# Kernel optimization log

Hardware: AMD Instinct MI355X
Metric: run time of the kernel (lower is better)

The kernel has to match this reference:

```python
import jax, jax.numpy as jnp
import numpy as np

HEADS = 6
EPS = 1e-5


def _na_idx(L, k, d):
    # NATTEN-style dilated neighborhood: work within dilation cosets,
    # clamp window to stay inside the image (window shifts at borders).
    i = np.arange(L)
    g = i % d
    p = i // d
    Lg = (L - g + d - 1) // d  # coset length per position
    start = np.clip(p - k // 2, 0, Lg - k)
    j = np.arange(k)
    nbr = g[:, None] + d * (start[:, None] + j[None, :])          # [L,k] neighbor coords
    rel = (start[:, None] + j[None, :]) - p[:, None] + (k - 1)    # [L,k] rpb index in [0,2k-2]
    return jnp.asarray(nbr, jnp.int32), jnp.asarray(rel, jnp.int32)


def _na2d(x, qkv_w, qkv_b, proj_w, proj_b, rpb, heads, k, d):
    # x: [B,H,W,C] NHWC neighborhood attention with relative positional bias
    B, H, W, C = x.shape
    dh = C // heads
    scale = dh ** -0.5
    qkv = (x @ qkv_w + qkv_b).reshape(B, H, W, 3, heads, dh)
    qkv = jnp.transpose(qkv, (3, 0, 4, 1, 2, 5))  # [3,B,h,H,W,dh]
    q, kk, v = qkv[0] * scale, qkv[1], qkv[2]
    nh, rh = _na_idx(H, k, d)
    nw, rw = _na_idx(W, k, d)

    def gather(t):  # [B,h,H,W,dh] -> [B,h,H,W,k,k,dh]
        t = t[:, :, nh]              # [B,h,H,k,W,dh]
        t = t[:, :, :, :, nw]        # [B,h,H,k,W,k,dh]
        return jnp.transpose(t, (0, 1, 2, 4, 3, 5, 6))

    kn, vn = gather(kk), gather(v)
    attn = jnp.einsum('bhxyd,bhxyijd->bhxyij', q, kn)  # [B,h,H,W,k,k]
    bias = rpb[:, rh]                  # [h,H,k,2k-1]
    bias = bias[:, :, :, rw]           # [h,H,k,W,k]
    bias = jnp.transpose(bias, (0, 1, 3, 2, 4))  # [h,H,W,k,k]
    attn = attn + bias[None]
    attn = jax.nn.softmax(attn.reshape(B, heads, H, W, k * k), axis=-1)
    attn = attn.reshape(B, heads, H, W, k, k)
    out = jnp.einsum('bhxyij,bhxyijd->bhxyd', attn, vn)
    out = jnp.transpose(out, (0, 2, 3, 1, 4)).reshape(B, H, W, C)
    return out @ proj_w + proj_b


def _rln(x, w, b, m1_w, m1_b, m2_w, m2_b):
    # Revised LayerNorm: normalize over (C,H,W) per sample; meta1/meta2 are 1x1 convs on std/mean
    mean = jnp.mean(x, axis=(1, 2, 3), keepdims=True)
    std = jnp.sqrt(jnp.mean((x - mean) ** 2, axis=(1, 2, 3), keepdims=True) + EPS)
    out = (x - mean) / std * w + b
    rescale = m1_w[None, :, None, None] * std + m1_b[None, :, None, None]
    rebias = m2_w[None, :, None, None] * mean + m2_b[None, :, None, None]
    return out, rescale, rebias


def _c11(x, w, b):  # 1x1 conv on NCHW == per-pixel linear
    return jnp.einsum('bchw,oc->bohw', x, w) + b[None, :, None, None]


def _gelu(x):
    return jax.nn.gelu(x, approximate=False)


def reference(x, ln_w, ln_b, m1_w, m1_b, m2_w, m2_b, qkv1_w, qkv1_b, proj1_w, proj1_b, rpb1, qkv2_w, qkv2_b, proj2_w, proj2_b, rpb2, mlp_w1, mlp_b1, mlp_w2, mlp_b2, bn_g, bn_b, bn_m, bn_v, pa_w1, pa_b1, pa_w2, pa_b2, ca_w1, ca_b1, ca_w2, ca_b2, m2a_w1, m2a_b1, m2a_w2, m2a_b2):
    # ---- NA block 1 (kernel 7, dilation 1) ----
    sc = x
    y, rs, rb = _rln(x, ln_w, ln_b, m1_w, m1_b, m2_w, m2_b)
    a = _na2d(jnp.transpose(y, (0, 2, 3, 1)), qkv1_w, qkv1_b, proj1_w, proj1_b, rpb1, HEADS, 7, 1)
    x = sc + jnp.transpose(a, (0, 3, 1, 2)) * rs + rb
    # ---- NA block 2 (kernel 5, dilation 8) ----
    sc = x
    y, rs, rb = _rln(x, ln_w, ln_b, m1_w, m1_b, m2_w, m2_b)
    a = _na2d(jnp.transpose(y, (0, 2, 3, 1)), qkv2_w, qkv2_b, proj2_w, proj2_b, rpb2, HEADS, 5, 8)
    x = sc + jnp.transpose(a, (0, 3, 1, 2)) * rs + rb
    # ---- MLP (source reuses the pre-attn2 shortcut `sc`) ----
    y, rs, rb = _rln(x, ln_w, ln_b, m1_w, m1_b, m2_w, m2_b)
    m = _c11(jax.nn.relu(_c11(y, mlp_w1, mlp_b1)), mlp_w2, mlp_b2)
    x = sc + m * rs + rb
    # ---- BN + pixel attention + channel attention + mlp2 ----
    sc = x
    inv = jax.lax.rsqrt(bn_v + EPS)
    y = (x - bn_m[None, :, None, None]) * (inv * bn_g)[None, :, None, None] + bn_b[None, :, None, None]
    pa = jax.nn.sigmoid(_c11(_gelu(_c11(y, pa_w1, pa_b1)), pa_w2, pa_b2))  # [B,1,H,W]
    y = pa * y
    gap = jnp.mean(y, axis=(2, 3), keepdims=True)
    ca = jax.nn.sigmoid(_c11(_gelu(_c11(gap, ca_w1, ca_b1)), ca_w2, ca_b2))  # [B,C,1,1]
    y = ca * y
    y = _c11(_gelu(_c11(y, m2a_w1, m2a_b1)), m2a_w2, m2a_b2)
    return sc + y


def setup_inputs() -> dict:
    key = jax.random.key(0)
    B, C, H, W, HID = 4, 96, 64, 64, 384
    ks = iter(jax.random.split(key, 48))

    def rn(shape, s=0.02):
        return jax.random.normal(next(ks), shape, jnp.float32) * s

    d = {}
    d['x'] = jax.random.normal(next(ks), (B, C, H, W), jnp.float32)
    d['ln_w'] = jnp.ones((1, C, 1, 1), jnp.float32)
    d['ln_b'] = jnp.zeros((1, C, 1, 1), jnp.float32)
    d['m1_w'] = rn((C,)); d['m1_b'] = jnp.ones((C,), jnp.float32)
    d['m2_w'] = rn((C,)); d['m2_b'] = jnp.zeros((C,), jnp.float32)
    d['qkv1_w'] = rn((C, 3 * C)); d['qkv1_b'] = jnp.zeros((3 * C,), jnp.float32)
    d['proj1_w'] = rn((C, C)); d['proj1_b'] = jnp.zeros((C,), jnp.float32)
    d['rpb1'] = rn((HEADS, 13, 13))
    d['qkv2_w'] = rn((C, 3 * C)); d['qkv2_b'] = jnp.zeros((3 * C,), jnp.float32)
    d['proj2_w'] = rn((C, C)); d['proj2_b'] = jnp.zeros((C,), jnp.float32)
    d['rpb2'] = rn((HEADS, 9, 9))
    d['mlp_w1'] = rn((HID, C)); d['mlp_b1'] = jnp.zeros((HID,), jnp.float32)
    d['mlp_w2'] = rn((C, HID)); d['mlp_b2'] = jnp.zeros((C,), jnp.float32)
    d['bn_g'] = jnp.ones((C,), jnp.float32); d['bn_b'] = jnp.zeros((C,), jnp.float32)
    d['bn_m'] = jnp.zeros((C,), jnp.float32); d['bn_v'] = jnp.ones((C,), jnp.float32)
    d['pa_w1'] = rn((C // 8, C)); d['pa_b1'] = jnp.zeros((C // 8,), jnp.float32)
    d['pa_w2'] = rn((1, C // 8)); d['pa_b2'] = jnp.zeros((1,), jnp.float32)
    d['ca_w1'] = rn((C, C)); d['ca_b1'] = jnp.zeros((C,), jnp.float32)
    d['ca_w2'] = rn((C, C)); d['ca_b2'] = jnp.zeros((C,), jnp.float32)
    d['m2a_w1'] = rn((C, C)); d['m2a_b1'] = jnp.zeros((C,), jnp.float32)
    d['m2a_w2'] = rn((C, C)); d['m2a_b2'] = jnp.zeros((C,), jnp.float32)
    return d
```

## Files before the change

### kernel.cpp

```cpp
#include <hip/hip_runtime.h>
#include <math.h>

#define CC 96
#define NP 4096
#define NHEADS 6
#define NELEMF 393216.0f
#define EPSF 1e-5f

typedef __attribute__((ext_vector_type(8))) short bf16x8;
typedef __attribute__((ext_vector_type(4))) float f32x4;
#define MFMA16(a,b,c) __builtin_amdgcn_mfma_f32_16x16x32_bf16(a,b,c,0,0,0)

#define WQKV1  64
#define WQKV2  (WQKV1+13824)
#define WPROJ1 (WQKV2+13824)
#define WPROJ2 (WPROJ1+4608)
#define WMLP1  (WPROJ2+4608)
#define WMLP2  (WMLP1+18432)
#define WM2A1  (WMLP2+18432)
#define WM2A2  (WM2A1+4608)
#define WPA1T  (WM2A2+4608)
#define WBNS   (WPA1T+1152)
#define WCA1T  (WBNS+192)
#define WCA2T  (WCA1T+9216)
#define WS_Q   870784
#define WS_K   (WS_Q+786432)
#define WS_V   (WS_K+786432)
#define WS_ATTPM (WS_V+786432)
#define WS_X1  (WS_ATTPM+786432)
#define WS_X2  (WS_X1+1572864)
#define WS_X3  (WS_X2+1572864)
#define WS_PA  (WS_X3+1572864)
#define WS_GAP (WS_PA+16384)

__device__ __forceinline__ float gelu_f(float x){
  return 0.5f * x * (1.0f + erff(x * 0.7071067811865476f));
}
__device__ __forceinline__ float sigmoid_f(float x){
  return 1.0f / (1.0f + __expf(-x));
}
__device__ __forceinline__ unsigned short bfr(float f){
  unsigned int u = __float_as_uint(f);
  u += 0x7fffu + ((u >> 16) & 1u);
  return (unsigned short)(u >> 16);
}
__device__ __forceinline__ float bflo16(unsigned short u){ return __uint_as_float(((unsigned int)u) << 16); }
__device__ __forceinline__ float bflo(unsigned int u){ return __uint_as_float(u << 16); }
__device__ __forceinline__ float bfhi(unsigned int u){ return __uint_as_float(u & 0xffff0000u); }
__device__ __forceinline__ void get_ms(const float* st, int b, float& mean, float& inv, float& stdv){
  float s = st[b], s2 = st[4+b];
  mean = s * (1.0f/NELEMF);
  float var = fmaxf(s2 * (1.0f/NELEMF) - mean*mean, 0.0f);
  stdv = sqrtf(var + EPSF);
  inv = 1.0f / stdv;
}
__device__ __forceinline__ float ldf(const float* p, int i){ return p[i]; }
__device__ __forceinline__ float ldf(const unsigned short* p, int i){ return bflo16(p[i]); }
__device__ __forceinline__ void load4(const float* p, float4& v){ v = *(const float4*)p; }
__device__ __forceinline__ void load4(const unsigned short* p, float4& v){
  ushort4 u = *(const ushort4*)p;
  v.x = bflo16(u.x); v.y = bflo16(u.y); v.z = bflo16(u.z); v.w = bflo16(u.w);
}

__global__ void prep_stats_kernel(const float* __restrict__ x, float* __restrict__ st,
                             const float* __restrict__ q1, const float* __restrict__ q2,
                             const float* __restrict__ p1, const float* __restrict__ p2,
                             const float* __restrict__ w1, const float* __restrict__ w2,
                             const float* __restrict__ a1, const float* __restrict__ a2,
                             const float* __restrict__ pw1,
                             const float* __restrict__ bg, const float* __restrict__ bb,
                             const float* __restrict__ bm, const float* __restrict__ bv,
                             const float* __restrict__ cw1, const float* __restrict__ cw2,
                             float* __restrict__ ws){
  if(blockIdx.x < 384){
    int b = blockIdx.x / CC, c = blockIdx.x % CC;
    const float* p = x + (b*CC + c)*NP;
    float s = 0.f, s2 = 0.f;
    for(int i = threadIdx.x; i < NP; i += 256){ float v = p[i]; s += v; s2 = fmaf(v, v, s2); }
    for(int off = 32; off > 0; off >>= 1){ s += __shfl_down(s, off); s2 += __shfl_down(s2, off); }
    __shared__ float ls[8];
    int wid = threadIdx.x >> 6;
    if((threadIdx.x & 63) == 0){ ls[wid] = s; ls[4+wid] = s2; }
    __syncthreads();
    if(threadIdx.x == 0){
      atomicAdd(&st[b],   ls[0]+ls[1]+ls[2]+ls[3]);
      atomicAdd(&st[4+b], ls[4]+ls[5]+ls[6]+ls[7]);
    }
    return;
  }
  int gid = (blockIdx.x - 384)*256 + threadIdx.x;
  if(gid < 27648){ int n = gid/96, c = gid%96; ((unsigned short*)(ws+WQKV1))[gid] = bfr(q1[c*288+n]); }
  else if(gid < 55296){ int g = gid-27648; int n = g/96, c = g%96; ((unsigned short*)(ws+WQKV2))[g] = bfr(q2[c*288+n]); }
  else if(gid < 64512){ int g = gid-55296; int n = g/96, c = g%96; ((unsigned short*)(ws+WPROJ1))[g] = bfr(p1[c*96+n]); }
  else if(gid < 73728){ int g = gid-64512; int n = g/96, c = g%96; ((unsigned short*)(ws+WPROJ2))[g] = bfr(p2[c*96+n]); }
  else if(gid < 110592){ int g = gid-73728; ((unsigned short*)(ws+WMLP1))[g] = bfr(w1[g]); }
  else if(gid < 147456){ int g = gid-110592; ((unsigned short*)(ws+WMLP2))[g] = bfr(w2[g]); }
  else if(gid < 156672){ int g = gid-147456; ((unsigned short*)(ws+WM2A1))[g] = bfr(a1[g]); }
  else if(gid < 165888){ int g = gid-156672; ((unsigned short*)(ws+WM2A2))[g] = bfr(a2[g]); }
  else if(gid < 167040){ int g = gid-165888; int c = g/12, h = g%12; ws[WPA1T + g] = pw1[h*96+c]; }
  else if(gid < 167136){ int c = gid-167040;
    float sc = rsqrtf(bv[c] + EPSF) * bg[c];
    ws[WBNS + c] = sc;
    ws[WBNS + 96 + c] = bb[c] - bm[c]*sc;
  }
  else if(gid < 167520){ ws[WS_GAP + (gid-167136)] = 0.f; }
  else if(gid < 176736){ int g = gid-167520; int o = g/96, c = g%96; ws[WCA1T + c*96 + o] = cw1[g]; }
  else if(gid < 185952){ int g = gid-176736; int o = g/96, c = g%96; ws[WCA2T + c*96 + o] = cw2[g]; }
}

template<typename AT>
__global__ void __launch_bounds__(256) gemm_qkv_kernel(
    const AT* __restrict__ xin, const float* __restrict__ st,
    const float* __restrict__ lnw, const float* __restrict__ lnb,
    const unsigned short* __restrict__ wT, const float* __restrict__ qb,
    unsigned short* __restrict__ qo, unsigned short* __restrict__ ko, unsigned short* __restrict__ vo){
  __shared__ unsigned short Atl[64*104];
  __shared__ float scl[96], ofs[96];
  int m_base = blockIdx.x*64;
  int b = m_base >> 12, pxl0 = m_base & 4095;
  float mean, inv, stdv; get_ms(st, b, mean, inv, stdv);
  int tid = threadIdx.x;
  if(tid < 96){ float s = inv*lnw[tid]; scl[tid] = s; ofs[tid] = lnb[tid] - mean*s; }
  __syncthreads();
  const AT* src = xin + (size_t)b*CC*NP + pxl0;
  for(int idx = tid; idx < 96*16; idx += 256){
    int c = idx >> 4, p4 = (idx & 15) << 2;
    float4 v; load4(src + (size_t)c*NP + p4, v);
    float s = scl[c], o = ofs[c];
    Atl[(p4+0)*104 + c] = bfr(fmaf(v.x, s, o));
    Atl[(p4+1)*104 + c] = bfr(fmaf(v.y, s, o));
    Atl[(p4+2)*104 + c] = bfr(fmaf(v.z, s, o));
    Atl[(p4+3)*104 + c] = bfr(fmaf(v.w, s, o));
  }
  __syncthreads();
  int w = tid >> 6, lane = tid & 63, ml = lane & 15, q = lane >> 4;
  const unsigned short* arow = Atl + (w*16 + ml)*104;
  bf16x8 av[3];
  #pragma unroll
  for(int ks = 0; ks < 3; ++ks) av[ks] = *(const bf16x8*)(arow + ks*32 + q*8);
  f32x4 z = {0.f,0.f,0.f,0.f};
  #pragma unroll
  for(int g = 0; g < 6; ++g){
    f32x4 acc[3] = {z, z, z};
    #pragma unroll
    for(int ks = 0; ks < 3; ++ks){
      #pragma unroll
      for(int gg = 0; gg < 3; ++gg){
        bf16x8 bv = *(const bf16x8*)(wT + (g*48 + gg*16 + ml)*96 + ks*32 + q*8);
        acc[gg] = MFMA16(av[ks], bv, acc[gg]);
      }
    }
    #pragma unroll
    for(int gg = 0; gg < 3; ++gg){
      int nfb = g*48 + gg*16;
      int t = nfb/96, head = (nfb%96) >> 4;
      float scale = (t == 0) ? 0.25f : 1.0f;
      unsigned short* dst = (t == 0) ? qo : (t == 1) ? ko : vo;
      float bias = qb[nfb + ml];
      #pragma unroll
      for(int r = 0; r < 4; ++r){
        int pxl = pxl0 + w*16 + q*4 + r;
        dst[(((size_t)(b*NHEADS + head))*NP + pxl)*16 + ml] = bfr((acc[gg][r] + bias)*scale);
      }
    }
  }
}

template<typename SCT>
__global__ void __launch_bounds__(256) gemm_proj_kernel(
    const unsigned short* __restrict__ attpm, const unsigned short* __restrict__ wT,
    const float* __restrict__ pb, const SCT* __restrict__ scx, const float* __restrict__ st,
    const float* __restrict__ m1w, const float* __restrict__ m1b,
    const float* __restrict__ m2w, const float* __restrict__ m2b,
    unsigned short* __restrict__ dst, float* __restrict__ st_out){
  int w = threadIdx.x >> 6, lane = threadIdx.x & 63;
  int ml = lane & 15, q = lane >> 4;
  int m_base = blockIdx.x*128 + w*32;
  int n0 = blockIdx.y*48;
  f32x4 acc[2][3];
  f32x4 z = {0.f,0.f,0.f,0.f};
  #pragma unroll
  for(int f=0; f<2; ++f) for(int g=0; g<3; ++g) acc[f][g] = z;
  {
    const bf16x8* a0 = (const bf16x8*)(attpm + (size_t)(m_base + ml)*96 + q*8);
    const bf16x8* a1 = (const bf16x8*)(attpm + (size_t)(m_base + 16 + ml)*96 + q*8);
    #pragma unroll
    for(int ks = 0; ks < 3; ++ks){
      bf16x8 av0 = a0[ks*4], av1 = a1[ks*4];
      #pragma unroll
      for(int g = 0; g < 3; ++g){
        bf16x8 bv = *(const bf16x8*)(wT + (n0 + g*16 + ml)*96 + ks*32 + q*8);
        acc[0][g] = MFMA16(av0, bv, acc[0][g]);
        acc[1][g] = MFMA16(av1, bv, acc[1][g]);
      }
    }
  }
  __shared__ float T[48*133];
  #pragma unroll
  for(int f = 0; f < 2; ++f)
    #pragma unroll
    for(int g = 0; g < 3; ++g)
      #pragma unroll
      for(int r = 0; r < 4; ++r)
        T[(g*16 + ml)*133 + w*32 + f*16 + q*4 + r] = acc[f][g][r];
  __syncthreads();
  int b = (blockIdx.x*128) >> 12, pxl0 = (blockIdx.x*128) & 4095;
  float mean, inv, stdv; get_ms(st, b, mean, inv, stdv);
  float s = 0.f, s2 = 0.f;
  for(int idx = threadIdx.x; idx < 48*128; idx += 256){
    int row = idx >> 7, px = idx & 127;
    int n = n0 + row;
    float rsf = fmaf(m1w[n], stdv, m1b[n]);
    float rbf = fmaf(m2w[n], mean, m2b[n]);
    int ad = (b*CC + n)*NP + pxl0 + px;
    float val = ldf(scx, ad) + (T[row*133 + px] + pb[n])*rsf + rbf;
    dst[ad] = bfr(val);
    s += val; s2 = fmaf(val, val, s2);
  }
  for(int off = 32; off > 0; off >>= 1){ s += __shfl_down(s, off); s2 += __shfl_down(s2, off); }
  __shared__ float ls[8];
  int wid = threadIdx.x >> 6;
  if((threadIdx.x & 63) == 0){ ls[wid] = s; ls[4+wid] = s2; }
  __syncthreads();
  if(threadIdx.x == 0){
    atomicAdd(&st_out[b],   ls[0]+ls[1]+ls[2]+ls[3]);
    atomicAdd(&st_out[4+b], ls[4]+ls[5]+ls[6]+ls[7]);
  }
}

__global__ void __launch_bounds__(256) gemm_mlp_kernel(
    const unsigned short* __restrict__ xin, const float* __restrict__ st,
    const float* __restrict__ lnw, const float* __restrict__ lnb,
    const unsigned short* __restrict__ w1T, const float* __restrict__ b1,
    const unsigned short* __restrict__ w2T, const float* __restrict__ b2,
    const unsigned short* __restrict__ scx,
    const float* __restrict__ m1w, const float* __restrict__ m1b,
    const float* __restrict__ m2w, const float* __restrict__ m2b,
    float* __restrict__ dst){
  __shared__ __align__(16) char smbuf[63488];
  __shared__ float scl[96], ofs[96];
  unsigned short* Atl  = (unsigned short*)smbuf;
  unsigned short* hidL = (unsigned short*)(smbuf + 13312);
  float* T = (float*)(smbuf + 13312);
  int m_base = blockIdx.x*64;
  int b = m_base >> 12, pxl0 = m_base & 4095;
  float mean, inv, stdv; get_ms(st, b, mean, inv, stdv);
  int tid = threadIdx.x;
  if(tid < 96){ float s = inv*lnw[tid]; scl[tid] = s; ofs[tid] = lnb[tid] - mean*s; }
  __syncthreads();
  const unsigned short* src = xin + (size_t)b*CC*NP + pxl0;
  for(int idx = tid; idx < 96*16; idx += 256){
    int c = idx >> 4, p4 = (idx & 15) << 2;
    float4 v; load4(src + (size_t)c*NP + p4, v);
    float s = scl[c], o = ofs[c];
    Atl[(p4+0)*104 + c] = bfr(fmaf(v.x, s, o));
    Atl[(p4+1)*104 + c] = bfr(fmaf(v.y, s, o));
    Atl[(p4+2)*104 + c] = bfr(fmaf(v.z, s, o));
    Atl[(p4+3)*104 + c] = bfr(fmaf(v.w, s, o));
  }
  __syncthreads();
  int w = tid >> 6, lane = tid & 63, ml = lane & 15, q = lane >> 4;
  f32x4 z = {0.f,0.f,0.f,0.f};
  {
    const unsigned short* arow = Atl + (w*16 + ml)*104;
    bf16x8 av[3];
    #pragma unroll
    for(int ks = 0; ks < 3; ++ks) av[ks] = *(const bf16x8*)(arow + ks*32 + q*8);
    #pragma unroll
    for(int g = 0; g < 8; ++g){
      f32x4 acc[3] = {z, z, z};
      #pragma unroll
      for(int ks = 0; ks < 3; ++ks){
        #pragma unroll
        for(int gg = 0; gg < 3; ++gg){
          bf16x8 bv = *(const bf16x8*)(w1T + (g*48 + gg*16 + ml)*96 + ks*32 + q*8);
          acc[gg] = MFMA16(av[ks], bv, acc[gg]);
        }
      }
      #pragma unroll
      for(int gg = 0; gg < 3; ++gg){
        int n = g*48 + gg*16 + ml;
        float bias = b1[n];
        #pragma unroll
        for(int r = 0; r < 4; ++r)
          hidL[(w*16 + q*4 + r)*392 + n] = bfr(fmaxf(acc[gg][r] + bias, 0.f));
      }
    }
  }
  __syncthreads();
  f32x4 acc2[6];
  #pragma unroll
  for(int g=0; g<6; ++g) acc2[g] = z;
  {
    const unsigned short* arow = hidL + (w*16 + ml)*392;
    #pragma unroll
    for(int ks = 0; ks < 12; ++ks){
      bf16x8 av = *(const bf16x8*)(arow + ks*32 + q*8);
      #pragma unroll
      for(int g = 0; g < 6; ++g){
        bf16x8 bv = *(const bf16x8*)(w2T + (g*16 + ml)*384 + ks*32 + q*8);
        acc2[g] = MFMA16(av, bv, acc2[g]);
      }
    }
  }
  __syncthreads();
  #pragma unroll
  for(int g = 0; g < 6; ++g)
    #pragma unroll
    for(int r = 0; r < 4; ++r)
      T[(g*16 + ml)*68 + w*16 + q*4 + r] = acc2[g][r];
  __syncthreads();
  for(int idx = tid; idx < 96*64; idx += 256){
    int n = idx >> 6, px = idx & 63;
    float rsf = fmaf(m1w[n], stdv, m1b[n]);
    float rbf = fmaf(m2w[n], mean, m2b[n]);
    int ad = (b*CC + n)*NP + pxl0 + px;
    dst[ad] = ldf(scx, ad) + (T[n*68 + px] + b2[n])*rsf + rbf;
  }
}

__global__ void __launch_bounds__(256) gemm_m2a_kernel(
    const float* __restrict__ x3, const float* __restrict__ bns,
    const float* __restrict__ pa, const float* __restrict__ gap,
    const float* __restrict__ cw1T, const float* __restrict__ cb1,
    const float* __restrict__ cw2T, const float* __restrict__ cb2,
    const unsigned short* __restrict__ w1T, const float* __restrict__ b1,
    const unsigned short* __restrict__ w2T, const float* __restrict__ b2,
    const float* __restrict__ scx, float* __restrict__ outp){
  __shared__ __align__(16) char smbuf[26624];
  __shared__ float scl[96], ofs[96], pal[64];
  __shared__ float gl[96], tl[96];
  unsigned short* Atl = (unsigned short*)smbuf;
  unsigned short* tl2 = (unsigned short*)(smbuf + 13312);
  float* T = (float*)smbuf;
  int m_base = blockIdx.x*64;
  int b = m_base >> 12, pxl0 = m_base & 4095;
  int tid = threadIdx.x;
  if(tid < 96) gl[tid] = gap[b*96 + tid];
  if(tid >= 128 && tid < 192) pal[tid-128] = pa[m_base + (tid-128)];
  __syncthreads();
  if(tid < 96){
    float a = cb1[tid];
    #pragma unroll 8
    for(int c = 0; c < 96; ++c) a = fmaf(gl[c], cw1T[c*96 + tid], a);
    tl[tid] = gelu_f(a);
  }
  __syncthreads();
  if(tid < 96){
    float a = cb2[tid];
    #pragma unroll 8
    for(int c = 0; c < 96; ++c) a = fmaf(tl[c], cw2T[c*96 + tid], a);
    float cv = sigmoid_f(a);
    scl[tid] = bns[tid]*cv; ofs[tid] = bns[96+tid]*cv;
  }
  __syncthreads();
  const float* src = x3 + (size_t)b*CC*NP + pxl0;
  for(int idx = tid; idx < 96*16; idx += 256){
    int c = idx >> 4, p4 = (idx & 15) << 2;
    float4 v = *(const float4*)(src + (size_t)c*NP + p4);
    float s = scl[c], o = ofs[c];
    Atl[(p4+0)*104 + c] = bfr(fmaf(v.x, s, o) * pal[p4+0]);
    Atl[(p4+1)*104 + c] = bfr(fmaf(v.y, s, o) * pal[p4+1]);
    Atl[(p4+2)*104 + c] = bfr(fmaf(v.z, s, o) * pal[p4+2]);
    Atl[(p4+3)*104 + c] = bfr(fmaf(v.w, s, o) * pal[p4+3]);
  }
  __syncthreads();
  int w = tid >> 6, lane = tid & 63, ml = lane & 15, q = lane >> 4;
  f32x4 z = {0.f,0.f,0.f,0.f};
  f32x4 acc1[6];
  #pragma unroll
  for(int g=0; g<6; ++g) acc1[g] = z;
  {
    const unsigned short* arow = Atl + (w*16 + ml)*104;
    #pragma unroll
    for(int ks = 0; ks < 3; ++ks){
      bf16x8 av = *(const bf16x8*)(arow + ks*32 + q*8);
      #pragma unroll
      for(int g = 0; g < 6; ++g){
        bf16x8 bv = *(const bf16x8*)(w1T + (g*16 + ml)*96 + ks*32 + q*8);
        acc1[g] = MFMA16(av, bv, acc1[g]);
      }
    }
  }
  #pragma unroll
  for(int g = 0; g < 6; ++g){
    float bias = b1[g*16 + ml];
    #pragma unroll
    for(int r = 0; r < 4; ++r)
      tl2[(w*16 + q*4 + r)*104 + g*16 + ml] = bfr(gelu_f(acc1[g][r] + bias));
  }
  __syncthreads();
  f32x4 acc2[6];
  #pragma unroll
  for(int g=0; g<6; ++g) acc2[g] = z;
  {
    const unsigned short* arow = tl2 + (w*16 + ml)*104;
    #pragma unroll
    for(int ks = 0; ks < 3; ++ks){
      bf16x8 av = *(const bf16x8*)(arow + ks*32 + q*8);
      #pragma unroll
      for(int g = 0; g < 6; ++g){
        bf16x8 bv = *(const bf16x8*)(w2T + (g*16 + ml)*96 + ks*32 + q*8);
        acc2[g] = MFMA16(av, bv, acc2[g]);
      }
    }
  }
  __syncthreads();
  #pragma unroll
  for(int g = 0; g < 6; ++g)
    #pragma unroll
    for(int r = 0; r < 4; ++r)
      T[(g*16 + ml)*68 + w*16 + q*4 + r] = acc2[g][r];
  __syncthreads();
  for(int idx = tid; idx < 96*64; idx += 256){
    int n = idx >> 6, p = idx & 63;
    int ad = (b*CC + n)*NP + pxl0 + p;
    outp[ad] = scx[ad] + T[n*68 + p] + b2[n];
  }
}

template<int K, int D, int RPB>
__global__ void __launch_bounds__(256) attn_kernel(
    const unsigned short* __restrict__ qb, const unsigned short* __restrict__ kb,
    const unsigned short* __restrict__ vb, const float* __restrict__ rpb,
    unsigned short* __restrict__ outp){
  int bh = blockIdx.x >> 6;
  int x = blockIdx.x & 63;
  int head = bh % NHEADS, b = bh / NHEADS;

  int gx = x % D, px = x / D;
  int Lgx = (64 - gx + D - 1) / D;
  int sx = min(max(px - K/2, 0), Lgx - K);

  __shared__ unsigned int sm[2*K*512];
  unsigned int* kl = sm;
  unsigned int* vl = sm + K*512;
  const unsigned int* kg = (const unsigned int*)(kb + (size_t)bh*NP*16);
  const unsigned int* vg = (const unsigned int*)(vb + (size_t)bh*NP*16);
  int tid = threadIdx.x;
  #pragma unroll
  for(int i = 0; i < K; ++i){
    int hh = gx + D*(sx + i);
    ((uint2*)(kl + i*512))[tid] = ((const uint2*)(kg + hh*512))[tid];
    ((uint2*)(vl + i*512))[tid] = ((const uint2*)(vg + hh*512))[tid];
  }
  __syncthreads();

  int pixoff = tid >> 2, t = tid & 3;
  int y = pixoff;
  int pix = x*64 + y;
  uint2 qd = *(const uint2*)(qb + ((size_t)bh*NP + pix)*16 + 4*t);
  float qx = bflo(qd.x), qy = bfhi(qd.x), qz = bflo(qd.y), qw = bfhi(qd.y);

  int gy = y % D, py = y / D;
  int Lgy = (64 - gy + D - 1) / D;
  int sy = min(max(py - K/2, 0), Lgy - K);

  float sc[K*K];
  #pragma unroll
  for(int i = 0; i < K; ++i){
    #pragma unroll
    for(int j = 0; j < K; ++j){
      int ww = gy + D*(sy + j);
      uint2 kv = *(const uint2*)(kl + i*512 + ww*8 + t*2);
      float s = qx*bflo(kv.x);
      s = fmaf(qy, bfhi(kv.x), s);
      s = fmaf(qz, bflo(kv.y), s);
      s = fmaf(qw, bfhi(kv.y), s);
      sc[i*K + j] = s;
    }
  }
  float mx = -1e30f;
  #pragma unroll
  for(int i = 0; i < K; ++i){
    const float* brow = rpb + (head*RPB + (sx + i - px + (K-1)))*RPB + (sy - py + (K-1));
    #pragma unroll
    for(int j = 0; j < K; ++j){
      float s = sc[i*K + j];
      s += __shfl_xor(s, 1);
      s += __shfl_xor(s, 2);
      s += brow[j];
      sc[i*K + j] = s;
      mx = fmaxf(mx, s);
    }
  }
  float sum = 0.f;
  #pragma unroll
  for(int n = 0; n < K*K; ++n){ float e = __expf(sc[n] - mx); sc[n] = e; sum += e; }
  float rs = 1.0f / sum;
  float4 acc = {0,0,0,0};
  #pragma unroll
  for(int i = 0; i < K; ++i){
    #pragma unroll
    for(int j = 0; j < K; ++j){
      int ww = gy + D*(sy + j);
      float wgt = sc[i*K + j] * rs;
      uint2 vv = *(const uint2*)(vl + i*512 + ww*8 + t*2);
      acc.x = fmaf(wgt, bflo(vv.x), acc.x);
      acc.y = fmaf(wgt, bfhi(vv.x), acc.y);
      acc.z = fmaf(wgt, bflo(vv.y), acc.z);
      acc.w = fmaf(wgt, bfhi(vv.y), acc.w);
    }
  }
  ushort4 o4;
  o4.x = bfr(acc.x); o4.y = bfr(acc.y); o4.z = bfr(acc.z); o4.w = bfr(acc.w);
  *(ushort4*)(outp + ((size_t)(b*NP + pix))*96 + head*16 + 4*t) = o4;
}

__global__ void __launch_bounds__(256) pa_gap_kernel(
    const float* __restrict__ x3, const float* __restrict__ bns,
    const float* __restrict__ w1t, const float* __restrict__ b1,
    const float* __restrict__ w2, const float* __restrict__ b2,
    float* __restrict__ pa, float* __restrict__ gap){
  int b = blockIdx.x >> 6;
  int px0 = (blockIdx.x & 63)*64;
  int pxq = threadIdx.x >> 2, t = threadIdx.x & 3;
  int p = px0 + pxq;
  float yvv[24];
  float acc[12];
  #pragma unroll
  for(int h = 0; h < 12; ++h) acc[h] = 0.f;
  #pragma unroll 6
  for(int cc = 0; cc < 24; ++cc){
    int c = t*24 + cc;
    float yv = fmaf(x3[(b*CC + c)*NP + p], bns[c], bns[96 + c]);
    yvv[cc] = yv;
    #pragma unroll
    for(int h = 0; h < 12; ++h) acc[h] = fmaf(yv, w1t[c*12 + h], acc[h]);
  }
  #pragma unroll
  for(int h = 0; h < 12; ++h){
    acc[h] += __shfl_xor(acc[h], 1);
    acc[h] += __shfl_xor(acc[h], 2);
  }
  float s = b2[0];
  #pragma unroll
  for(int h = 0; h < 12; ++h) s = fmaf(gelu_f(acc[h] + b1[h]), w2[h], s);
  float pav = sigmoid_f(s);
  if(t == 0) pa[b*NP + p] = pav;
  __shared__ float gpart[4*96];
  int w = threadIdx.x >> 6, lane = threadIdx.x & 63;
  #pragma unroll 6
  for(int cc = 0; cc < 24; ++cc){
    float g = yvv[cc] * pav;
    g += __shfl_xor(g, 4);  g += __shfl_xor(g, 8);
    g += __shfl_xor(g, 16); g += __shfl_xor(g, 32);
    if(lane < 4 && lane == t) gpart[w*96 + t*24 + cc] = g;
  }
  __syncthreads();
  if(threadIdx.x < 96){
    int c = threadIdx.x;
    float v = (gpart[c] + gpart[96+c] + gpart[192+c] + gpart[288+c]) * (1.0f/4096.0f);
    atomicAdd(&gap[b*96 + c], v);
  }
}

extern "C" void kernel_launch(void* const* d_in, const int* in_sizes, int n_in,
                              void* d_out, int out_size, void* d_ws, size_t ws_size,
                              hipStream_t stream){
  (void)in_sizes; (void)n_in; (void)out_size; (void)ws_size;
  const float* x     = (const float*)d_in[0];
  const float* lnw   = (const float*)d_in[1];
  const float* lnb   = (const float*)d_in[2];
  const float* m1w   = (const float*)d_in[3];
  const float* m1b   = (const float*)d_in[4];
  const float* m2w   = (const float*)d_in[5];
  const float* m2b   = (const float*)d_in[6];
  const float* qkv1w = (const float*)d_in[7];
  const float* qkv1b = (const float*)d_in[8];
  const float* proj1w= (const float*)d_in[9];
  const float* proj1b= (const float*)d_in[10];
  const float* rpb1  = (const float*)d_in[11];
  const float* qkv2w = (const float*)d_in[12];
  const float* qkv2b = (const float*)d_in[13];
  const float* proj2w= (const float*)d_in[14];
  const float* proj2b= (const float*)d_in[15];
  const float* rpb2  = (const float*)d_in[16];
  const float* mw1   = (const float*)d_in[17];
  const float* mb1   = (const float*)d_in[18];
  const float* mw2   = (const float*)d_in[19];
  const float* mb2   = (const float*)d_in[20];
  const float* bng   = (const float*)d_in[21];
  const float* bnb   = (const float*)d_in[22];
  const float* bnm   = (const float*)d_in[23];
  const float* bnv   = (const float*)d_in[24];
  const float* paw1  = (const float*)d_in[25];
  const float* pab1  = (const float*)d_in[26];
  const float* paw2  = (const float*)d_in[27];
  const float* pab2  = (const float*)d_in[28];
  const float* caw1  = (const float*)d_in[29];
  const float* cab1  = (const float*)d_in[30];
  const float* caw2  = (const float*)d_in[31];
  const float* cab2  = (const float*)d_in[32];
  const float* aw1   = (const float*)d_in[33];
  const float* ab1   = (const float*)d_in[34];
  const float* aw2   = (const float*)d_in[35];
  const float* ab2   = (const float*)d_in[36];

  float* ws  = (float*)d_ws;
  float* out = (float*)d_out;
  float* st0 = ws;
  float* st1 = ws + 8;
  float* st2 = ws + 16;
  unsigned short* q     = (unsigned short*)(ws + WS_Q);
  unsigned short* k     = (unsigned short*)(ws + WS_K);
  unsigned short* v     = (unsigned short*)(ws + WS_V);
  unsigned short* attpm = (unsigned short*)(ws + WS_ATTPM);
  unsigned short* x1b   = (unsigned short*)(ws + WS_X1);
  unsigned short* x2b   = (unsigned short*)(ws + WS_X2);
  float* x3  = ws + WS_X3;
  float* pab = ws + WS_PA;
  float* gpb = ws + WS_GAP;
  float* bns = ws + WBNS;

  hipMemsetAsync(d_ws, 0, 64*sizeof(float), stream);
  prep_stats_kernel<<<1111, 256, 0, stream>>>(x, st0, qkv1w, qkv2w, proj1w, proj2w,
                                              mw1, mw2, aw1, aw2, paw1,
                                              bng, bnb, bnm, bnv, caw1, caw2, ws);

  gemm_qkv_kernel<float><<<256, 256, 0, stream>>>(x, st0, lnw, lnb,
      (unsigned short*)(ws+WQKV1), qkv1b, q, k, v);
  attn_kernel<7,1,13><<<1536, 256, 0, stream>>>(q, k, v, rpb1, attpm);
  gemm_proj_kernel<float><<<dim3(128,2), 256, 0, stream>>>(attpm, (unsigned short*)(ws+WPROJ1),
      proj1b, x, st0, m1w, m1b, m2w, m2b, x1b, st1);

  gemm_qkv_kernel<unsigned short><<<256, 256, 0, stream>>>(x1b, st1, lnw, lnb,
      (unsigned short*)(ws+WQKV2), qkv2b, q, k, v);
  attn_kernel<5,8,9><<<1536, 256, 0, stream>>>(q, k, v, rpb2, attpm);
  gemm_proj_kernel<unsigned short><<<dim3(128,2), 256, 0, stream>>>(attpm, (unsigned short*)(ws+WPROJ2),
      proj2b, x1b, st1, m1w, m1b, m2w, m2b, x2b, st2);

  gemm_mlp_kernel<<<256, 256, 0, stream>>>(x2b, st2, lnw, lnb,
      (unsigned short*)(ws+WMLP1), mb1, (unsigned short*)(ws+WMLP2), mb2,
      x1b, m1w, m1b, m2w, m2b, x3);

  pa_gap_kernel<<<256, 256, 0, stream>>>(x3, bns, ws + WPA1T, pab1, paw2, pab2, pab, gpb);
  gemm_m2a_kernel<<<256, 256, 0, stream>>>(x3, bns, pab, gpb,
                                           ws + WCA1T, cab1, ws + WCA2T, cab2,
                                           (unsigned short*)(ws+WM2A1), ab1,
                                           (unsigned short*)(ws+WM2A2), ab2, x3, out);
}
```

Measured before the change: 287.6 us.

## Double threads per block in GEMM and pa_gap kernels, vectorize stats reduction

Raises the block size from 256 to 512 threads for the QKV, proj, MLP, m2a and pa_gap kernels and splits each block's output columns or channels across the extra waves, so each wave does half the MFMA work. This targets poor latency hiding, since with only 256 blocks most of the hardware sits idle. The stats pass in prep_stats now reads float4 instead of scalar floats. In exchange, A-tile loads are duplicated across wave pairs and reduction and shared-memory bookkeeping grows.

```diff
diff --git a/kernel.cpp b/kernel.cpp
--- a/kernel.cpp
+++ b/kernel.cpp
@@ -74,9 +74,13 @@
                              float* __restrict__ ws){
   if(blockIdx.x < 384){
     int b = blockIdx.x / CC, c = blockIdx.x % CC;
-    const float* p = x + (b*CC + c)*NP;
+    const float4* p4 = (const float4*)(x + (size_t)(b*CC + c)*NP);
     float s = 0.f, s2 = 0.f;
-    for(int i = threadIdx.x; i < NP; i += 256){ float v = p[i]; s += v; s2 = fmaf(v, v, s2); }
+    for(int i = threadIdx.x; i < 1024; i += 256){
+      float4 v = p4[i];
+      s += v.x + v.y + v.z + v.w;
+      s2 = fmaf(v.x, v.x, fmaf(v.y, v.y, fmaf(v.z, v.z, fmaf(v.w, v.w, s2))));
+    }
     for(int off = 32; off > 0; off >>= 1){ s += __shfl_down(s, off); s2 += __shfl_down(s2, off); }
     __shared__ float ls[8];
     int wid = threadIdx.x >> 6;
@@ -109,7 +113,7 @@
 }
 
 template<typename AT>
-__global__ void __launch_bounds__(256) gemm_qkv_kernel(
+__global__ void __launch_bounds__(512) gemm_qkv_kernel(
     const AT* __restrict__ xin, const float* __restrict__ st,
     const float* __restrict__ lnw, const float* __restrict__ lnb,
     const unsigned short* __restrict__ wT, const float* __restrict__ qb,
@@ -123,7 +127,7 @@
   if(tid < 96){ float s = inv*lnw[tid]; scl[tid] = s; ofs[tid] = lnb[tid] - mean*s; }
   __syncthreads();
   const AT* src = xin + (size_t)b*CC*NP + pxl0;
-  for(int idx = tid; idx < 96*16; idx += 256){
+  for(int idx = tid; idx < 96*16; idx += 512){
     int c = idx >> 4, p4 = (idx & 15) << 2;
     float4 v; load4(src + (size_t)c*NP + p4, v);
     float s = scl[c], o = ofs[c];
@@ -134,13 +138,15 @@
   }
   __syncthreads();
   int w = tid >> 6, lane = tid & 63, ml = lane & 15, q = lane >> 4;
-  const unsigned short* arow = Atl + (w*16 + ml)*104;
+  int row = w & 3, nh = w >> 2;
+  const unsigned short* arow = Atl + (row*16 + ml)*104;
   bf16x8 av[3];
   #pragma unroll
   for(int ks = 0; ks < 3; ++ks) av[ks] = *(const bf16x8*)(arow + ks*32 + q*8);
   f32x4 z = {0.f,0.f,0.f,0.f};
   #pragma unroll
-  for(int g = 0; g < 6; ++g){
+  for(int g0 = 0; g0 < 3; ++g0){
+    int g = nh*3 + g0;
     f32x4 acc[3] = {z, z, z};
     #pragma unroll
     for(int ks = 0; ks < 3; ++ks){
@@ -159,7 +165,7 @@
       float bias = qb[nfb + ml];
       #pragma unroll
       for(int r = 0; r < 4; ++r){
-        int pxl = pxl0 + w*16 + q*4 + r;
+        int pxl = pxl0 + row*16 + q*4 + r;
         dst[(((size_t)(b*NHEADS + head))*NP + pxl)*16 + ml] = bfr((acc[gg][r] + bias)*scale);
       }
     }
@@ -167,7 +173,7 @@
 }
 
 template<typename SCT>
-__global__ void __launch_bounds__(256) gemm_proj_kernel(
+__global__ void __launch_bounds__(512) gemm_proj_kernel(
     const unsigned short* __restrict__ attpm, const unsigned short* __restrict__ wT,
     const float* __restrict__ pb, const SCT* __restrict__ scx, const float* __restrict__ st,
     const float* __restrict__ m1w, const float* __restrict__ m1b,
@@ -175,39 +181,33 @@
     unsigned short* __restrict__ dst, float* __restrict__ st_out){
   int w = threadIdx.x >> 6, lane = threadIdx.x & 63;
   int ml = lane & 15, q = lane >> 4;
-  int m_base = blockIdx.x*128 + w*32;
+  int m_base = blockIdx.x*128 + w*16;
   int n0 = blockIdx.y*48;
-  f32x4 acc[2][3];
   f32x4 z = {0.f,0.f,0.f,0.f};
-  #pragma unroll
-  for(int f=0; f<2; ++f) for(int g=0; g<3; ++g) acc[f][g] = z;
+  f32x4 acc[3] = {z, z, z};
   {
     const bf16x8* a0 = (const bf16x8*)(attpm + (size_t)(m_base + ml)*96 + q*8);
-    const bf16x8* a1 = (const bf16x8*)(attpm + (size_t)(m_base + 16 + ml)*96 + q*8);
     #pragma unroll
     for(int ks = 0; ks < 3; ++ks){
-      bf16x8 av0 = a0[ks*4], av1 = a1[ks*4];
+      bf16x8 av0 = a0[ks*4];
       #pragma unroll
       for(int g = 0; g < 3; ++g){
         bf16x8 bv = *(const bf16x8*)(wT + (n0 + g*16 + ml)*96 + ks*32 + q*8);
-        acc[0][g] = MFMA16(av0, bv, acc[0][g]);
-        acc[1][g] = MFMA16(av1, bv, acc[1][g]);
+        acc[g] = MFMA16(av0, bv, acc[g]);
       }
     }
   }
   __shared__ float T[48*133];
   #pragma unroll
-  for(int f = 0; f < 2; ++f)
-    #pragma unroll
-    for(int g = 0; g < 3; ++g)
-      #pragma unroll
-      for(int r = 0; r < 4; ++r)
-        T[(g*16 + ml)*133 + w*32 + f*16 + q*4 + r] = acc[f][g][r];
+  for(int g = 0; g < 3; ++g)
+    #pragma unroll
+    for(int r = 0; r < 4; ++r)
+      T[(g*16 + ml)*133 + w*16 + q*4 + r] = acc[g][r];
   __syncthreads();
   int b = (blockIdx.x*128) >> 12, pxl0 = (blockIdx.x*128) & 4095;
   float mean, inv, stdv; get_ms(st, b, mean, inv, stdv);
   float s = 0.f, s2 = 0.f;
-  for(int idx = threadIdx.x; idx < 48*128; idx += 256){
+  for(int idx = threadIdx.x; idx < 48*128; idx += 512){
     int row = idx >> 7, px = idx & 127;
     int n = n0 + row;
     float rsf = fmaf(m1w[n], stdv, m1b[n]);
@@ -218,17 +218,17 @@
     s += val; s2 = fmaf(val, val, s2);
   }
   for(int off = 32; off > 0; off >>= 1){ s += __shfl_down(s, off); s2 += __shfl_down(s2, off); }
-  __shared__ float ls[8];
+  __shared__ float ls[16];
   int wid = threadIdx.x >> 6;
-  if((threadIdx.x & 63) == 0){ ls[wid] = s; ls[4+wid] = s2; }
+  if((threadIdx.x & 63) == 0){ ls[wid] = s; ls[8+wid] = s2; }
   __syncthreads();
   if(threadIdx.x == 0){
-    atomicAdd(&st_out[b],   ls[0]+ls[1]+ls[2]+ls[3]);
-    atomicAdd(&st_out[4+b], ls[4]+ls[5]+ls[6]+ls[7]);
-  }
-}
-
-__global__ void __launch_bounds__(256) gemm_mlp_kernel(
+    atomicAdd(&st_out[b],   ls[0]+ls[1]+ls[2]+ls[3]+ls[4]+ls[5]+ls[6]+ls[7]);
+    atomicAdd(&st_out[4+b], ls[8]+ls[9]+ls[10]+ls[11]+ls[12]+ls[13]+ls[14]+ls[15]);
+  }
+}
+
+__global__ void __launch_bounds__(512) gemm_mlp_kernel(
     const unsigned short* __restrict__ xin, const float* __restrict__ st,
     const float* __restrict__ lnw, const float* __restrict__ lnb,
     const unsigned short* __restrict__ w1T, const float* __restrict__ b1,
@@ -249,7 +249,7 @@
   if(tid < 96){ float s = inv*lnw[tid]; scl[tid] = s; ofs[tid] = lnb[tid] - mean*s; }
   __syncthreads();
   const unsigned short* src = xin + (size_t)b*CC*NP + pxl0;
-  for(int idx = tid; idx < 96*16; idx += 256){
+  for(int idx = tid; idx < 96*16; idx += 512){
     int c = idx >> 4, p4 = (idx & 15) << 2;
     float4 v; load4(src + (size_t)c*NP + p4, v);
     float s = scl[c], o = ofs[c];
@@ -260,14 +260,16 @@
   }
   __syncthreads();
   int w = tid >> 6, lane = tid & 63, ml = lane & 15, q = lane >> 4;
+  int row = w & 3, nh = w >> 2;
   f32x4 z = {0.f,0.f,0.f,0.f};
   {
-    const unsigned short* arow = Atl + (w*16 + ml)*104;
+    const unsigned short* arow = Atl + (row*16 + ml)*104;
     bf16x8 av[3];
     #pragma unroll
     for(int ks = 0; ks < 3; ++ks) av[ks] = *(const bf16x8*)(arow + ks*32 + q*8);
     #pragma unroll
-    for(int g = 0; g < 8; ++g){
+    for(int g0 = 0; g0 < 4; ++g0){
+      int g = nh*4 + g0;
       f32x4 acc[3] = {z, z, z};
       #pragma unroll
       for(int ks = 0; ks < 3; ++ks){
@@ -283,34 +285,35 @@
         float bias = b1[n];
         #pragma unroll
         for(int r = 0; r < 4; ++r)
-          hidL[(w*16 + q*4 + r)*392 + n] = bfr(fmaxf(acc[gg][r] + bias, 0.f));
-      }
-    }
-  }
-  __syncthreads();
-  f32x4 acc2[6];
-  #pragma unroll
-  for(int g=0; g<6; ++g) acc2[g] = z;
+          hidL[(row*16 + q*4 + r)*392 + n] = bfr(fmaxf(acc[gg][r] + bias, 0.f));
+      }
+    }
+  }
+  __syncthreads();
+  f32x4 acc2[3] = {z, z, z};
   {
-    const unsigned short* arow = hidL + (w*16 + ml)*392;
+    const unsigned short* arow = hidL + (row*16 + ml)*392;
     #pragma unroll
     for(int ks = 0; ks < 12; ++ks){
       bf16x8 av = *(const bf16x8*)(arow + ks*32 + q*8);
       #pragma unroll
-      for(int g = 0; g < 6; ++g){
+      for(int g0 = 0; g0 < 3; ++g0){
+        int g = nh*3 + g0;
         bf16x8 bv = *(const bf16x8*)(w2T + (g*16 + ml)*384 + ks*32 + q*8);
-        acc2[g] = MFMA16(av, bv, acc2[g]);
-      }
-    }
-  }
-  __syncthreads();
-  #pragma unroll
-  for(int g = 0; g < 6; ++g)
+        acc2[g0] = MFMA16(av, bv, acc2[g0]);
+      }
+    }
+  }
+  __syncthreads();
+  #pragma unroll
+  for(int g0 = 0; g0 < 3; ++g0){
+    int g = nh*3 + g0;
     #pragma unroll
     for(int r = 0; r < 4; ++r)
-      T[(g*16 + ml)*68 + w*16 + q*4 + r] = acc2[g][r];
-  __syncthreads();
-  for(int idx = tid; idx < 96*64; idx += 256){
+      T[(g*16 + ml)*68 + row*16 + q*4 + r] = acc2[g0][r];
+  }
+  __syncthreads();
+  for(int idx = tid; idx < 96*64; idx += 512){
     int n = idx >> 6, px = idx & 63;
     float rsf = fmaf(m1w[n], stdv, m1b[n]);
     float rbf = fmaf(m2w[n], mean, m2b[n]);
@@ -319,7 +322,7 @@
   }
 }
 
-__global__ void __launch_bounds__(256) gemm_m2a_kernel(
+__global__ void __launch_bounds__(512) gemm_m2a_kernel(
     const float* __restrict__ x3, const float* __restrict__ bns,
     const float* __restrict__ pa, const float* __restrict__ gap,
     const float* __restrict__ cw1T, const float* __restrict__ cb1,
@@ -355,7 +358,7 @@
   }
   __syncthreads();
   const float* src = x3 + (size_t)b*CC*NP + pxl0;
-  for(int idx = tid; idx < 96*16; idx += 256){
+  for(int idx = tid; idx < 96*16; idx += 512){
     int c = idx >> 4, p4 = (idx & 15) << 2;
     float4 v = *(const float4*)(src + (size_t)c*NP + p4);
     float s = scl[c], o = ofs[c];
@@ -366,53 +369,55 @@
   }
   __syncthreads();
   int w = tid >> 6, lane = tid & 63, ml = lane & 15, q = lane >> 4;
+  int row = w & 3, nh = w >> 2;
   f32x4 z = {0.f,0.f,0.f,0.f};
-  f32x4 acc1[6];
-  #pragma unroll
-  for(int g=0; g<6; ++g) acc1[g] = z;
+  f32x4 acc1[3] = {z, z, z};
   {
-    const unsigned short* arow = Atl + (w*16 + ml)*104;
+    const unsigned short* arow = Atl + (row*16 + ml)*104;
     #pragma unroll
     for(int ks = 0; ks < 3; ++ks){
       bf16x8 av = *(const bf16x8*)(arow + ks*32 + q*8);
       #pragma unroll
-      for(int g = 0; g < 6; ++g){
+      for(int g0 = 0; g0 < 3; ++g0){
+        int g = nh*3 + g0;
         bf16x8 bv = *(const bf16x8*)(w1T + (g*16 + ml)*96 + ks*32 + q*8);
-        acc1[g] = MFMA16(av, bv, acc1[g]);
-      }
-    }
-  }
-  #pragma unroll
-  for(int g = 0; g < 6; ++g){
+        acc1[g0] = MFMA16(av, bv, acc1[g0]);
+      }
+    }
+  }
+  #pragma unroll
+  for(int g0 = 0; g0 < 3; ++g0){
+    int g = nh*3 + g0;
     float bias = b1[g*16 + ml];
     #pragma unroll
     for(int r = 0; r < 4; ++r)
-      tl2[(w*16 + q*4 + r)*104 + g*16 + ml] = bfr(gelu_f(acc1[g][r] + bias));
-  }
-  __syncthreads();
-  f32x4 acc2[6];
-  #pragma unroll
-  for(int g=0; g<6; ++g) acc2[g] = z;
+      tl2[(row*16 + q*4 + r)*104 + g*16 + ml] = bfr(gelu_f(acc1[g0][r] + bias));
+  }
+  __syncthreads();
+  f32x4 acc2[3] = {z, z, z};
   {
-    const unsigned short* arow = tl2 + (w*16 + ml)*104;
+    const unsigned short* arow = tl2 + (row*16 + ml)*104;
     #pragma unroll
     for(int ks = 0; ks < 3; ++ks){
       bf16x8 av = *(const bf16x8*)(arow + ks*32 + q*8);
       #pragma unroll
-      for(int g = 0; g < 6; ++g){
+      for(int g0 = 0; g0 < 3; ++g0){
+        int g = nh*3 + g0;
         bf16x8 bv = *(const bf16x8*)(w2T + (g*16 + ml)*96 + ks*32 + q*8);
-        acc2[g] = MFMA16(av, bv, acc2[g]);
-      }
-    }
-  }
-  __syncthreads();
-  #pragma unroll
-  for(int g = 0; g < 6; ++g)
+        acc2[g0] = MFMA16(av, bv, acc2[g0]);
+      }
+    }
+  }
+  __syncthreads();
+  #pragma unroll
+  for(int g0 = 0; g0 < 3; ++g0){
+    int g = nh*3 + g0;
     #pragma unroll
     for(int r = 0; r < 4; ++r)
-      T[(g*16 + ml)*68 + w*16 + q*4 + r] = acc2[g][r];
-  __syncthreads();
-  for(int idx = tid; idx < 96*64; idx += 256){
+      T[(g*16 + ml)*68 + row*16 + q*4 + r] = acc2[g0][r];
+  }
+  __syncthreads();
+  for(int idx = tid; idx < 96*64; idx += 512){
     int n = idx >> 6, p = idx & 63;
     int ad = (b*CC + n)*NP + pxl0 + p;
     outp[ad] = scx[ad] + T[n*68 + p] + b2[n];
@@ -507,22 +512,22 @@
   *(ushort4*)(outp + ((size_t)(b*NP + pix))*96 + head*16 + 4*t) = o4;
 }
 
-__global__ void __launch_bounds__(256) pa_gap_kernel(
+__global__ void __launch_bounds__(512) pa_gap_kernel(
     const float* __restrict__ x3, const float* __restrict__ bns,
     const float* __restrict__ w1t, const float* __restrict__ b1,
     const float* __restrict__ w2, const float* __restrict__ b2,
     float* __restrict__ pa, float* __restrict__ gap){
   int b = blockIdx.x >> 6;
   int px0 = (blockIdx.x & 63)*64;
-  int pxq = threadIdx.x >> 2, t = threadIdx.x & 3;
+  int pxq = threadIdx.x >> 3, t = threadIdx.x & 7;
   int p = px0 + pxq;
-  float yvv[24];
+  float yvv[12];
   float acc[12];
   #pragma unroll
   for(int h = 0; h < 12; ++h) acc[h] = 0.f;
   #pragma unroll 6
-  for(int cc = 0; cc < 24; ++cc){
-    int c = t*24 + cc;
+  for(int cc = 0; cc < 12; ++cc){
+    int c = t*12 + cc;
     float yv = fmaf(x3[(b*CC + c)*NP + p], bns[c], bns[96 + c]);
     yvv[cc] = yv;
     #pragma unroll
@@ -532,26 +537,28 @@
   for(int h = 0; h < 12; ++h){
     acc[h] += __shfl_xor(acc[h], 1);
     acc[h] += __shfl_xor(acc[h], 2);
+    acc[h] += __shfl_xor(acc[h], 4);
   }
   float s = b2[0];
   #pragma unroll
   for(int h = 0; h < 12; ++h) s = fmaf(gelu_f(acc[h] + b1[h]), w2[h], s);
   float pav = sigmoid_f(s);
   if(t == 0) pa[b*NP + p] = pav;
-  __shared__ float gpart[4*96];
+  __shared__ float gpart[8*96];
   int w = threadIdx.x >> 6, lane = threadIdx.x & 63;
   #pragma unroll 6
-  for(int cc = 0; cc < 24; ++cc){
+  for(int cc = 0; cc < 12; ++cc){
     float g = yvv[cc] * pav;
-    g += __shfl_xor(g, 4);  g += __shfl_xor(g, 8);
-    g += __shfl_xor(g, 16); g += __shfl_xor(g, 32);
-    if(lane < 4 && lane == t) gpart[w*96 + t*24 + cc] = g;
+    g += __shfl_xor(g, 8);  g += __shfl_xor(g, 16); g += __shfl_xor(g, 32);
+    if(lane < 8) gpart[w*96 + lane*12 + cc] = g;
   }
   __syncthreads();
   if(threadIdx.x < 96){
     int c = threadIdx.x;
-    float v = (gpart[c] + gpart[96+c] + gpart[192+c] + gpart[288+c]) * (1.0f/4096.0f);
-    atomicAdd(&gap[b*96 + c], v);
+    float v = 0.f;
+    #pragma unroll
+    for(int ww = 0; ww < 8; ++ww) v += gpart[ww*96 + c];
+    atomicAdd(&gap[b*96 + c], v * (1.0f/4096.0f));
   }
 }
 
@@ -618,24 +625,24 @@
                                               mw1, mw2, aw1, aw2, paw1,
                                               bng, bnb, bnm, bnv, caw1, caw2, ws);
 
-  gemm_qkv_kernel<float><<<256, 256, 0, stream>>>(x, st0, lnw, lnb,
+  gemm_qkv_kernel<float><<<256, 512, 0, stream>>>(x, st0, lnw, lnb,
       (unsigned short*)(ws+WQKV1), qkv1b, q, k, v);
   attn_kernel<7,1,13><<<1536, 256, 0, stream>>>(q, k, v, rpb1, attpm);
-  gemm_proj_kernel<float><<<dim3(128,2), 256, 0, stream>>>(attpm, (unsigned short*)(ws+WPROJ1),
+  gemm_proj_kernel<float><<<dim3(128,2), 512, 0, stream>>>(attpm, (unsigned short*)(ws+WPROJ1),
       proj1b, x, st0, m1w, m1b, m2w, m2b, x1b, st1);
 
-  gemm_qkv_kernel<unsigned short><<<256, 256, 0, stream>>>(x1b, st1, lnw, lnb,
+  gemm_qkv_kernel<unsigned short><<<256, 512, 0, stream>>>(x1b, st1, lnw, lnb,
       (unsigned short*)(ws+WQKV2), qkv2b, q, k, v);
   attn_kernel<5,8,9><<<1536, 256, 0, stream>>>(q, k, v, rpb2, attpm);
-  gemm_proj_kernel<unsigned short><<<dim3(128,2), 256, 0, stream>>>(attpm, (unsigned short*)(ws+WPROJ2),
+  gemm_proj_kernel<unsigned short><<<dim3(128,2), 512, 0, stream>>>(attpm, (unsigned short*)(ws+WPROJ2),
       proj2b, x1b, st1, m1w, m1b, m2w, m2b, x2b, st2);
 
-  gemm_mlp_kernel<<<256, 256, 0, stream>>>(x2b, st2, lnw, lnb,
+  gemm_mlp_kernel<<<256, 512, 0, stream>>>(x2b, st2, lnw, lnb,
       (unsigned short*)(ws+WMLP1), mb1, (unsigned short*)(ws+WMLP2), mb2,
       x1b, m1w, m1b, m2w, m2b, x3);
 
-  pa_gap_kernel<<<256, 256, 0, stream>>>(x3, bns, ws + WPA1T, pab1, paw2, pab2, pab, gpb);
-  gemm_m2a_kernel<<<256, 256, 0, stream>>>(x3, bns, pab, gpb,
+  pa_gap_kernel<<<256, 512, 0, stream>>>(x3, bns, ws + WPA1T, pab1, paw2, pab2, pab, gpb);
+  gemm_m2a_kernel<<<256, 512, 0, stream>>>(x3, bns, pab, gpb,
                                            ws + WCA1T, cab1, ws + WCA2T, cab2,
                                            (unsigned short*)(ws+WM2A1), ab1,
                                            (unsigned short*)(ws+WM2A2), ab2, x3, out);
```

After: 274.3 us. 1.05x faster.
